# Optimization experiments

Measured on AMD Instinct MI355X. Metric: run time of the kernel, lower is better.

Reference implementation:

```python
import jax, jax.numpy as jnp
import numpy as np

B, S, D, H, DH, F = 2, 2048, 1024, 16, 64, 4096
EPS = 1e-5


def layernorm(x, gamma, beta):
    mu = jnp.mean(x, axis=-1, keepdims=True)
    var = jnp.mean((x - mu) ** 2, axis=-1, keepdims=True)
    return (x - mu) * jax.lax.rsqrt(var + EPS) * gamma + beta


def setup_inputs() -> dict:
    key = jax.random.key(0)
    ks = jax.random.split(key, 13)
    sc = 0.02
    return {
        "x": jax.random.normal(ks[0], (B, S, D), jnp.float32),
        "W_Q": jax.random.normal(ks[1], (H, DH, D), jnp.float32) * sc,  # per-head [d_head, d_model]
        "W_K": jax.random.normal(ks[2], (H, DH, D), jnp.float32) * sc,
        "W_V": jax.random.normal(ks[3], (H, DH, D), jnp.float32) * sc,
        "W_O": jax.random.normal(ks[4], (H * DH, D), jnp.float32) * sc,
        "W_up": jax.random.normal(ks[5], (D, F), jnp.float32) * sc,
        "b_up": jax.random.normal(ks[6], (F,), jnp.float32) * sc,
        "W_down": jax.random.normal(ks[7], (F, D), jnp.float32) * sc,
        "b_down": jax.random.normal(ks[8], (D,), jnp.float32) * sc,
        "gamma_1": jnp.ones((D,), jnp.float32),
        "beta_1": jnp.zeros((D,), jnp.float32),
        "gamma_2": jnp.ones((D,), jnp.float32),
        "beta_2": jnp.zeros((D,), jnp.float32),
    }


def reference(x, W_Q, W_K, W_V, W_O, W_up, b_up, W_down, b_down, gamma_1, beta_1, gamma_2, beta_2):
    u = layernorm(x, gamma_1, beta_1)
    # per-head projections: input @ W.t() -> [B, H, S, DH]
    Q = jnp.einsum("bsd,hed->bhse", u, W_Q)
    K = jnp.einsum("bsd,hed->bhse", u, W_K)
    V = jnp.einsum("bsd,hed->bhse", u, W_V)
    # Faithful quirk: original does K.reshape(B, DH, S) (raw reshape, NOT transpose)
    K_r = K.reshape(B, H, DH, S)
    scores = jnp.matmul(Q, K_r) / D  # [B,H,S,S]; quirk: scaled by d_model, not sqrt(d_head)
    attn = jax.nn.softmax(scores, axis=-1)
    heads = jnp.matmul(attn, V)  # [B,H,S,DH]
    heads_cat = heads.transpose(0, 2, 1, 3).reshape(B, S, H * DH)  # concat heads on last dim
    z1 = x + heads_cat @ W_O
    v1 = layernorm(z1, gamma_2, beta_2)
    v3 = jax.nn.gelu(v1 @ W_up + b_up, approximate=False)
    z2 = z1 + v3 @ W_down + b_down
    return z2
```

## Files before the change

### kernel.cpp

```cpp
#include <hip/hip_runtime.h>
#include <hip/hip_bf16.h>


typedef __attribute__((ext_vector_type(8))) short short8v;
typedef __attribute__((ext_vector_type(4))) short short4v;
typedef __attribute__((ext_vector_type(4))) float f32x4;

__device__ __forceinline__ float b2f(unsigned short u) {
    unsigned int x = ((unsigned int)u) << 16;
    float f;
    __builtin_memcpy(&f, &x, 4);
    return f;
}
__device__ __forceinline__ unsigned short f2b(float f) {
    unsigned int x;
    __builtin_memcpy(&x, &f, 4);
    unsigned int r = (x + 0x7FFFu + ((x >> 16) & 1u)) >> 16;
    return (unsigned short)r;
}
__device__ __forceinline__ void gload16(const unsigned short* g, unsigned short* l) {
    __builtin_amdgcn_global_load_lds(
        (const __attribute__((address_space(1))) unsigned int*)g,
        (__attribute__((address_space(3))) unsigned int*)l, 16, 0, 0);
}
__device__ __forceinline__ bool is_f32(const unsigned int* flagp) {
    return *flagp == 0x3F800000u;
}

__global__ __launch_bounds__(256) void cast_qkv_k(const void* __restrict__ s0,
                                                  const void* __restrict__ s1,
                                                  const void* __restrict__ s2,
                                                  unsigned short* __restrict__ dst,
                                                  const unsigned int* __restrict__ flagp) {
    const bool f32 = is_f32(flagp);
    const int seg = blockIdx.x >> 9;
    const int i = ((blockIdx.x & 511) * 256 + threadIdx.x) * 8;
    const void* src = seg == 0 ? s0 : (seg == 1 ? s1 : s2);
    unsigned short* d = dst + (size_t)seg * 1048576 + i;
    if (f32) {
        const float* s = (const float*)src + i;
        float4 a = *(const float4*)s;
        float4 b = *(const float4*)(s + 4);
        union { unsigned short u[8]; int4 v; } o;
        o.u[0] = f2b(a.x); o.u[1] = f2b(a.y); o.u[2] = f2b(a.z); o.u[3] = f2b(a.w);
        o.u[4] = f2b(b.x); o.u[5] = f2b(b.y); o.u[6] = f2b(b.z); o.u[7] = f2b(b.w);
        *(int4*)d = o.v;
    } else {
        *(int4*)d = *(const int4*)((const unsigned short*)src + i);
    }
}

__global__ __launch_bounds__(256) void cast_small_k(const void* __restrict__ s0,
                                                    const void* __restrict__ s1,
                                                    const void* __restrict__ s2,
                                                    const void* __restrict__ s3,
                                                    const void* __restrict__ s4,
                                                    const void* __restrict__ s5,
                                                    unsigned short* __restrict__ dst,
                                                    const unsigned int* __restrict__ flagp) {
    const bool f32 = is_f32(flagp);
    const int seg = blockIdx.x < 2 ? 0 : blockIdx.x - 1;
    const void* srcs[6] = {s0, s1, s2, s3, s4, s5};
    const int offs[6] = {0, 4096, 5120, 6144, 7168, 8192};
    const int lens[6] = {4096, 1024, 1024, 1024, 1024, 1024};
    const int base = (blockIdx.x < 2 ? blockIdx.x * 2048 : 0);
    const int i = base + threadIdx.x * 8;
    if (i >= lens[seg]) return;
    const void* src = srcs[seg];
    unsigned short* d = dst + offs[seg] + i;
    if (f32) {
        const float* s = (const float*)src + i;
        float4 a = *(const float4*)s;
        float4 b = *(const float4*)(s + 4);
        union { unsigned short u[8]; int4 v; } o;
        o.u[0] = f2b(a.x); o.u[1] = f2b(a.y); o.u[2] = f2b(a.z); o.u[3] = f2b(a.w);
        o.u[4] = f2b(b.x); o.u[5] = f2b(b.y); o.u[6] = f2b(b.z); o.u[7] = f2b(b.w);
        *(int4*)d = o.v;
    } else {
        *(int4*)d = *(const int4*)((const unsigned short*)src + i);
    }
}

__global__ __launch_bounds__(256) void castT_k(const void* __restrict__ src,
                                               unsigned short* __restrict__ dst,
                                               int rows, int cols,
                                               const unsigned int* __restrict__ flagp) {
    const bool f32 = is_f32(flagp);
    __shared__ float tile[32][33];
    const int t = threadIdx.x, tx = t & 31, ty = t >> 5;
    const int c0 = blockIdx.x * 32, r0 = blockIdx.y * 32;
#pragma unroll
    for (int i = 0; i < 4; i++) {
        int r = r0 + ty + i * 8;
        float v;
        if (f32) v = ((const float*)src)[(size_t)r * cols + c0 + tx];
        else     v = b2f(((const unsigned short*)src)[(size_t)r * cols + c0 + tx]);
        tile[ty + i * 8][tx] = v;
    }
    __syncthreads();
#pragma unroll
    for (int i = 0; i < 4; i++) {
        int c = c0 + ty + i * 8;
        dst[(size_t)c * rows + r0 + tx] = f2b(tile[tx][ty + i * 8]);
    }
}

__global__ __launch_bounds__(256) void kvT_k(const unsigned short* __restrict__ Kn,
                                             const unsigned short* __restrict__ Vn,
                                             unsigned short* __restrict__ Ktt,
                                             unsigned short* __restrict__ Vtt) {
    __shared__ unsigned short tile[64][72];
    const int blk = blockIdx.x;
    const int bh = blk >> 6;
    const int sub = blk & 63;
    const size_t base = (size_t)bh * (2048 * 64);
    const unsigned short* src;
    unsigned short* dst;
    int R, C, r0, c0;
    if (sub < 32) { src = Kn + base; dst = Ktt + base; R = 64;   C = 2048; r0 = 0;              c0 = sub * 64; }
    else          { src = Vn + base; dst = Vtt + base; R = 2048; C = 64;   r0 = (sub - 32) * 64; c0 = 0; }
    const int t = threadIdx.x;
    const int tx = t & 7, ty = t >> 3;
#pragma unroll
    for (int i = 0; i < 2; i++) {
        int r = ty + i * 32;
        union { int4 v; unsigned short u[8]; } ld;
        ld.v = *(const int4*)&src[(size_t)(r0 + r) * C + c0 + tx * 8];
#pragma unroll
        for (int k = 0; k < 8; k++) tile[tx * 8 + k][r] = ld.u[k];
    }
    __syncthreads();
#pragma unroll
    for (int i = 0; i < 2; i++) {
        int c = ty + i * 32;
        union { int4 v; unsigned short u[8]; } stv;
#pragma unroll
        for (int k = 0; k < 8; k++) stv.u[k] = tile[c][tx * 8 + k];
        *(int4*)&dst[(size_t)(c0 + c) * R + r0 + tx * 8] = stv.v;
    }
}

__global__ __launch_bounds__(256) void fin_k(const float* __restrict__ src,
                                             const unsigned short* __restrict__ P0,
                                             const unsigned short* __restrict__ P1,
                                             void* __restrict__ dst,
                                             const unsigned short* __restrict__ bias,
                                             const unsigned int* __restrict__ flagp) {
    const bool f32 = is_f32(flagp);
    const int i = (blockIdx.x * 256 + threadIdx.x) * 4;
    float4 v = *(const float4*)(src + i);
    uint2 p0 = *(const uint2*)(P0 + i);
    uint2 p1 = *(const uint2*)(P1 + i);
    int c = i & 1023;
    v.x += b2f(bias[c])     + b2f((unsigned short)(p0.x & 0xffff)) + b2f((unsigned short)(p1.x & 0xffff));
    v.y += b2f(bias[c + 1]) + b2f((unsigned short)(p0.x >> 16))    + b2f((unsigned short)(p1.x >> 16));
    v.z += b2f(bias[c + 2]) + b2f((unsigned short)(p0.y & 0xffff)) + b2f((unsigned short)(p1.y & 0xffff));
    v.w += b2f(bias[c + 3]) + b2f((unsigned short)(p0.y >> 16))    + b2f((unsigned short)(p1.y >> 16));
    if (f32) {
        *(float4*)((float*)dst + i) = v;
    } else {
        union { unsigned short u[4]; uint2 q; } o;
        o.u[0] = f2b(v.x); o.u[1] = f2b(v.y); o.u[2] = f2b(v.z); o.u[3] = f2b(v.w);
        *(uint2*)((unsigned short*)dst + i) = o.q;
    }
}

template <int MODE>
__global__ __launch_bounds__(256) void ln_k(const void* __restrict__ inp,
                                            unsigned short* __restrict__ outp,
                                            const unsigned short* __restrict__ gamma,
                                            const unsigned short* __restrict__ beta,
                                            const unsigned int* __restrict__ flagp) {
    const int row = blockIdx.x, t = threadIdx.x;
    float xv[4];
    bool f32 = (MODE == 1) ? true : is_f32(flagp);
    if (f32) {
        const float* p = (const float*)inp + (size_t)row * 1024 + t * 4;
        float4 v = *(const float4*)p;
        xv[0] = v.x; xv[1] = v.y; xv[2] = v.z; xv[3] = v.w;
    } else {
        const unsigned short* p = (const unsigned short*)inp + (size_t)row * 1024 + t * 4;
        uint2 v = *(const uint2*)p;
        xv[0] = b2f((unsigned short)(v.x & 0xffff));
        xv[1] = b2f((unsigned short)(v.x >> 16));
        xv[2] = b2f((unsigned short)(v.y & 0xffff));
        xv[3] = b2f((unsigned short)(v.y >> 16));
    }
    float s = xv[0] + xv[1] + xv[2] + xv[3];
    float q = xv[0] * xv[0] + xv[1] * xv[1] + xv[2] * xv[2] + xv[3] * xv[3];
#pragma unroll
    for (int off = 32; off >= 1; off >>= 1) {
        s += __shfl_xor(s, off);
        q += __shfl_xor(q, off);
    }
    __shared__ float ls[8];
    if ((t & 63) == 0) { ls[t >> 6] = s; ls[4 + (t >> 6)] = q; }
    __syncthreads();
    s = ls[0] + ls[1] + ls[2] + ls[3];
    q = ls[4] + ls[5] + ls[6] + ls[7];
    const float mu = s * (1.f / 1024.f);
    const float rs = rsqrtf(q * (1.f / 1024.f) - mu * mu + 1e-5f);
    union { unsigned short u[4]; uint2 v; } o;
#pragma unroll
    for (int i = 0; i < 4; i++) {
        int c = t * 4 + i;
        o.u[i] = f2b((xv[i] - mu) * rs * b2f(gamma[c]) + b2f(beta[c]));
    }
    *(uint2*)(outp + (size_t)row * 1024 + t * 4) = o.v;
}

template <int EPI>
__global__ __launch_bounds__(256) void gemm_k(const unsigned short* __restrict__ A,
                                              const unsigned short* __restrict__ Bm,
                                              unsigned short* __restrict__ C,
                                              unsigned short* __restrict__ C2,
                                              unsigned short* __restrict__ C3,
                                              const unsigned short* __restrict__ bias,
                                              float* __restrict__ outf,
                                              const void* __restrict__ xres,
                                              const unsigned int* __restrict__ flagp,
                                              int N, int ldk, int tilesM, int tilesN,
                                              int kLen) {
    __shared__ unsigned short As[2][128 * 32];
    __shared__ unsigned short Bs[2][128 * 32];
    const int t = threadIdx.x;
    const int w = t >> 6, lane = t & 63, ln = t & 15, quad = (t & 63) >> 4;
    const int wm = w >> 1, wn = w & 1;
    const int bm = blockIdx.x % tilesM;
    const int bn = (blockIdx.x / tilesM) % tilesN;
    const int kc = blockIdx.x / (tilesM * tilesN);
    const int m0 = bm << 7, n0 = bn << 7;
    const int k0 = kc * kLen;
    f32x4 acc[4][4] = {};

    const int srow = lane >> 2;
    const int scol = (lane & 3) << 3;

    const size_t arow[2] = {(size_t)(m0 + (0 * 4 + w) * 16 + srow) * ldk + scol,
                            (size_t)(m0 + (1 * 4 + w) * 16 + srow) * ldk + scol};
    const size_t brow[2] = {(size_t)(n0 + (0 * 4 + w) * 16 + srow) * ldk + scol,
                            (size_t)(n0 + (1 * 4 + w) * 16 + srow) * ldk + scol};

#pragma unroll
    for (int r = 0; r < 2; r++) {
        const int blk = r * 4 + w;
        gload16(&A[arow[r] + k0], &As[0][blk * 512]);
        gload16(&Bm[brow[r] + k0], &Bs[0][blk * 512]);
    }

    int cur = 0;
    for (int kt = k0; kt < k0 + kLen; kt += 32) {
        asm volatile("s_waitcnt vmcnt(0)" ::: "memory");
        __syncthreads();
        if (kt + 32 < k0 + kLen) {
#pragma unroll
            for (int r = 0; r < 2; r++) {
                const int blk = r * 4 + w;
                gload16(&A[arow[r] + kt + 32], &As[cur ^ 1][blk * 512]);
                gload16(&Bm[brow[r] + kt + 32], &Bs[cur ^ 1][blk * 512]);
            }
        }
        short8v af[4], bfv[4];
#pragma unroll
        for (int mi = 0; mi < 4; mi++)
            af[mi] = *(const short8v*)&As[cur][(wm * 64 + mi * 16 + ln) * 32 + quad * 8];
#pragma unroll
        for (int nj = 0; nj < 4; nj++)
            bfv[nj] = *(const short8v*)&Bs[cur][(wn * 64 + nj * 16 + ln) * 32 + quad * 8];
#pragma unroll
        for (int mi = 0; mi < 4; mi++)
#pragma unroll
            for (int nj = 0; nj < 4; nj++)
                acc[mi][nj] = __builtin_amdgcn_mfma_f32_16x16x32_bf16(
                    af[mi], bfv[nj], acc[mi][nj], 0, 0, 0);
        cur ^= 1;
    }

    bool xf32 = false;
    if (EPI == 3) xf32 = is_f32(flagp);
    unsigned short* Cp = C;
    if (EPI == 8) Cp = C + (size_t)kc * 4194304;

#pragma unroll
    for (int mi = 0; mi < 4; mi++) {
#pragma unroll
        for (int nj = 0; nj < 4; nj++) {
#pragma unroll
            for (int r = 0; r < 4; r++) {
                const int m = m0 + wm * 64 + mi * 16 + quad * 4 + r;
                const int n = n0 + wn * 64 + nj * 16 + ln;
                float v = acc[mi][nj][r];
                if (EPI == 3) {
                    float xv = xf32 ? ((const float*)xres)[(size_t)m * N + n]
                                    : b2f(((const unsigned short*)xres)[(size_t)m * N + n]);
                    outf[(size_t)m * N + n] = v + xv;
                } else if (EPI == 4) {
                    float x = v + b2f(bias[n]);
                    C[(size_t)m * N + n] = f2b(0.5f * x * (1.f + erff(x * 0.70710678118654752f)));
                } else if (EPI == 6) {
                    int b = m >> 11, s = m & 2047;
                    int seg = n >> 10, nn = n & 1023, h = nn >> 6, e = nn & 63;
                    size_t off = ((size_t)(b * 16 + h) * 2048 + s) * 64 + e;
                    if (seg == 0)      C[off]  = f2b(v);
                    else if (seg == 1) C2[off] = f2b(v);
                    else               C3[off] = f2b(v);
                } else {
                    Cp[(size_t)m * N + n] = f2b(v);
                }
            }
        }
    }
}

__global__ __launch_bounds__(512, 4) void attn_k(const unsigned short* __restrict__ Q,
                                                 const unsigned short* __restrict__ Kt,
                                                 const unsigned short* __restrict__ Vt,
                                                 unsigned short* __restrict__ Hd) {
    __shared__ unsigned short Ks[2][2][128 * 32];
    __shared__ unsigned short Vs[2][64 * 128];
    const int t = threadIdx.x;
    const int w = t >> 6, l = t & 63, ln = t & 15, quad = (t & 63) >> 4;
    const int qt = blockIdx.x & 15, bh = blockIdx.x >> 4;
    const int b = bh >> 4, h = bh & 15;
    const int i0 = qt << 7;

    short8v aq[2];
    {
        const unsigned short* qp =
            Q + ((size_t)bh * 2048 + i0 + w * 16 + ln) * 64 + quad * 8;
        aq[0] = *(const short8v*)qp;
        aq[1] = *(const short8v*)(qp + 32);
    }

    const size_t kbase = (size_t)bh * (2048 * 64);
    const size_t vbase = (size_t)bh * (64 * 2048);

    size_t ksrc[2]; int klds[2];
    size_t vsrc[2]; int vlds[2];
#pragma unroll
    for (int r = 0; r < 2; r++) {
        int idx2 = w * 2 + r;
        int ksp = idx2 & 1, J = idx2 >> 1;
        ksrc[r] = (size_t)(J * 16 + (l >> 2)) * 64 + ksp * 32 + (l & 3) * 8;
        klds[r] = ksp * 4096 + J * 512;
        int c = idx2;
        int e = c * 4 + (l >> 4), pp = l & 15;
        int g = (pp & 8) | ((pp & 7) ^ (e & 7));
        vsrc[r] = (size_t)e * 2048 + g * 8;
        vlds[r] = c * 512;
    }

#pragma unroll
    for (int r = 0; r < 2; r++) {
        gload16(Kt + kbase + ksrc[r], &Ks[0][0][0] + klds[r]);
        gload16(Vt + vbase + vsrc[r], &Vs[0][0] + vlds[r]);
    }

    f32x4 O[4] = {};
    float lsum = 0.f;
    int cur = 0;
    const float sc = 9.765625e-4f;

    for (int jt = 0; jt < 16; jt++) {
        asm volatile("s_waitcnt vmcnt(0)" ::: "memory");
        __syncthreads();
        if (jt < 15) {
            const size_t j1 = (size_t)(jt + 1) << 7;
#pragma unroll
            for (int r = 0; r < 2; r++) {
                gload16(Kt + kbase + j1 * 64 + ksrc[r], &Ks[cur ^ 1][0][0] + klds[r]);
                gload16(Vt + vbase + j1 + vsrc[r], &Vs[cur ^ 1][0] + vlds[r]);
            }
        }

        f32x4 S[8] = {};
#pragma unroll
        for (int ks = 0; ks < 2; ks++) {
#pragma unroll
            for (int nj = 0; nj < 8; nj++) {
                short8v bk = *(const short8v*)&Ks[cur][ks][(nj * 16 + ln) * 32 + quad * 8];
                S[nj] = __builtin_amdgcn_mfma_f32_16x16x32_bf16(bk, aq[ks], S[nj], 0, 0, 0);
            }
        }
        short4v pk[8];
#pragma unroll
        for (int nj = 0; nj < 8; nj++) {
            union { unsigned short u[4]; short4v v; } pu;
#pragma unroll
            for (int r = 0; r < 4; r++) {
                float p = __expf(S[nj][r] * sc);
                lsum += p;
                pu.u[r] = f2b(p);
            }
            pk[nj] = pu.v;
        }
#pragma unroll
        for (int nj = 0; nj < 8; nj++) {
            int g = 2 * nj + (quad >> 1);
            int pos = (g & 8) | ((g & 7) ^ (ln & 7));
            int off = pos * 8 + (quad & 1) * 4;
#pragma unroll
            for (int ne = 0; ne < 4; ne++) {
                short4v bv = *(const short4v*)&Vs[cur][(ne * 16 + ln) * 128 + off];
                O[ne] = __builtin_amdgcn_mfma_f32_16x16x16bf16_1k(pk[nj], bv, O[ne], 0, 0, 0);
            }
        }
        cur ^= 1;
    }

    lsum += __shfl_xor(lsum, 16);
    lsum += __shfl_xor(lsum, 32);

#pragma unroll
    for (int r = 0; r < 4; r++) {
        float lr = __shfl(lsum, quad * 4 + r);
        float inv = 1.f / lr;
#pragma unroll
        for (int ne = 0; ne < 4; ne++) {
            int i = i0 + w * 16 + quad * 4 + r;
            int e = ne * 16 + ln;
            Hd[((size_t)(b * 2048 + i)) * 1024 + h * 64 + e] = f2b(O[ne][r] * inv);
        }
    }
}

extern "C" void kernel_launch(void* const* d_in, const int* in_sizes, int n_in,
                              void* d_out, int out_size, void* d_ws, size_t ws_size,
                              hipStream_t stream) {
    const unsigned int* flagp = (const unsigned int*)d_in[9];

    unsigned short* p = (unsigned short*)d_ws;
    unsigned short* Wqkv  = p; p += 3145728;
    unsigned short* WOt   = p; p += 1048576;
    unsigned short* Wupt  = p; p += 4194304;
    unsigned short* Wdnt  = p; p += 4194304;
    unsigned short* smallv = p; p += 9216;
    unsigned short* u     = p; p += 4194304;
    unsigned short* Qn    = p; p += 4194304;
    unsigned short* Kn    = p; p += 4194304;
    unsigned short* Vn    = p; p += 4194304;
    unsigned short* Ktt   = p; p += 4194304;
    unsigned short* Vtt   = p; p += 4194304;
    unsigned short* hd    = p; p += 4194304;
    float*          z1    = (float*)p;
    unsigned short* bupc = smallv;
    unsigned short* bdnc = smallv + 4096;
    unsigned short* g1c  = smallv + 5120;
    unsigned short* be1c = smallv + 6144;
    unsigned short* g2c  = smallv + 7168;
    unsigned short* be2c = smallv + 8192;
    unsigned short* v1   = u;
    unsigned short* v3   = Qn;
    unsigned short* Pd   = Wqkv;

    dim3 blk(256);
    cast_qkv_k<<<1536, blk, 0, stream>>>(d_in[1], d_in[2], d_in[3], Wqkv, flagp);
    castT_k<<<dim3(32, 32),  blk, 0, stream>>>(d_in[4], WOt,  1024, 1024, flagp);
    castT_k<<<dim3(128, 32), blk, 0, stream>>>(d_in[5], Wupt, 1024, 4096, flagp);
    castT_k<<<dim3(32, 128), blk, 0, stream>>>(d_in[7], Wdnt, 4096, 1024, flagp);
    cast_small_k<<<7, blk, 0, stream>>>(d_in[6], d_in[8], d_in[9], d_in[10], d_in[11],
                                        d_in[12], smallv, flagp);

    ln_k<0><<<4096, blk, 0, stream>>>(d_in[0], u, g1c, be1c, flagp);
    gemm_k<6><<<768, blk, 0, stream>>>(u, Wqkv, Qn, Kn, Vn, nullptr, nullptr,
                                       nullptr, nullptr, 3072, 1024, 32, 24, 1024);
    kvT_k<<<2048, blk, 0, stream>>>(Kn, Vn, Ktt, Vtt);
    attn_k<<<512, dim3(512), 0, stream>>>(Qn, Ktt, Vtt, hd);
    gemm_k<3><<<256, blk, 0, stream>>>(hd, WOt, nullptr, nullptr, nullptr, nullptr, z1,
                                       d_in[0], flagp, 1024, 1024, 32, 8, 1024);
    ln_k<1><<<4096, blk, 0, stream>>>(z1, v1, g2c, be2c, flagp);
    gemm_k<4><<<1024, blk, 0, stream>>>(v1, Wupt, v3, nullptr, nullptr, bupc, nullptr,
                                        nullptr, nullptr, 4096, 1024, 32, 32, 1024);
    gemm_k<8><<<512, blk, 0, stream>>>(v3, Wdnt, Pd, nullptr, nullptr, nullptr, nullptr,
                                       nullptr, nullptr, 1024, 4096, 32, 8, 2048);
    fin_k<<<4096, blk, 0, stream>>>(z1, Pd, Pd + 4194304, d_out, bdnc, flagp);
}
```

Baseline: 412.8 us.

## Add 256x256-tile GEMM with 4-stage LDS pipeline for QKV, up and down projections

Adds a new gemm256_k kernel with 512 threads and 256x256 output tiles. It uses a 4-buffer direct-to-LDS prefetch ring with explicit waitcnt and barrier scheduling, swizzled LDS reads, and raised wave priority around the MFMA blocks. It replaces the 128x128 GEMMs for the QKV, FFN-up and FFN-down projections to raise data reuse per tile. The down projection now splits K four ways instead of two, so fin_k sums four bf16 partial buffers that reuse dead scratch regions. The costs are lower grid counts (192–256 blocks) and higher LDS and register pressure, with a risk of poor CU fill.

```diff
diff --git a/kernel.cpp b/kernel.cpp
--- a/kernel.cpp
+++ b/kernel.cpp
@@ -143,6 +143,8 @@
 __global__ __launch_bounds__(256) void fin_k(const float* __restrict__ src,
                                              const unsigned short* __restrict__ P0,
                                              const unsigned short* __restrict__ P1,
+                                             const unsigned short* __restrict__ P2,
+                                             const unsigned short* __restrict__ P3,
                                              void* __restrict__ dst,
                                              const unsigned short* __restrict__ bias,
                                              const unsigned int* __restrict__ flagp) {
@@ -151,11 +153,17 @@
     float4 v = *(const float4*)(src + i);
     uint2 p0 = *(const uint2*)(P0 + i);
     uint2 p1 = *(const uint2*)(P1 + i);
+    uint2 p2 = *(const uint2*)(P2 + i);
+    uint2 p3 = *(const uint2*)(P3 + i);
     int c = i & 1023;
-    v.x += b2f(bias[c])     + b2f((unsigned short)(p0.x & 0xffff)) + b2f((unsigned short)(p1.x & 0xffff));
-    v.y += b2f(bias[c + 1]) + b2f((unsigned short)(p0.x >> 16))    + b2f((unsigned short)(p1.x >> 16));
-    v.z += b2f(bias[c + 2]) + b2f((unsigned short)(p0.y & 0xffff)) + b2f((unsigned short)(p1.y & 0xffff));
-    v.w += b2f(bias[c + 3]) + b2f((unsigned short)(p0.y >> 16))    + b2f((unsigned short)(p1.y >> 16));
+    v.x += b2f(bias[c])     + b2f((unsigned short)(p0.x & 0xffff)) + b2f((unsigned short)(p1.x & 0xffff))
+                            + b2f((unsigned short)(p2.x & 0xffff)) + b2f((unsigned short)(p3.x & 0xffff));
+    v.y += b2f(bias[c + 1]) + b2f((unsigned short)(p0.x >> 16))    + b2f((unsigned short)(p1.x >> 16))
+                            + b2f((unsigned short)(p2.x >> 16))    + b2f((unsigned short)(p3.x >> 16));
+    v.z += b2f(bias[c + 2]) + b2f((unsigned short)(p0.y & 0xffff)) + b2f((unsigned short)(p1.y & 0xffff))
+                            + b2f((unsigned short)(p2.y & 0xffff)) + b2f((unsigned short)(p3.y & 0xffff));
+    v.w += b2f(bias[c + 3]) + b2f((unsigned short)(p0.y >> 16))    + b2f((unsigned short)(p1.y >> 16))
+                            + b2f((unsigned short)(p2.y >> 16))    + b2f((unsigned short)(p3.y >> 16));
     if (f32) {
         *(float4*)((float*)dst + i) = v;
     } else {
@@ -278,8 +286,6 @@
 
     bool xf32 = false;
     if (EPI == 3) xf32 = is_f32(flagp);
-    unsigned short* Cp = C;
-    if (EPI == 8) Cp = C + (size_t)kc * 4194304;
 
 #pragma unroll
     for (int mi = 0; mi < 4; mi++) {
@@ -294,9 +300,133 @@
                     float xv = xf32 ? ((const float*)xres)[(size_t)m * N + n]
                                     : b2f(((const unsigned short*)xres)[(size_t)m * N + n]);
                     outf[(size_t)m * N + n] = v + xv;
-                } else if (EPI == 4) {
+                }
+            }
+        }
+    }
+}
+
+template <int EPI>
+__global__ __launch_bounds__(512, 2) void gemm256_k(const unsigned short* __restrict__ A,
+                                                    const unsigned short* __restrict__ Bm,
+                                                    unsigned short* __restrict__ C,
+                                                    unsigned short* __restrict__ C2,
+                                                    unsigned short* __restrict__ C3,
+                                                    const unsigned short* __restrict__ bias,
+                                                    int N, int ldk, int tilesM, int tilesN,
+                                                    int kLen) {
+    __shared__ unsigned short As[4][8192];
+    __shared__ unsigned short Bs[4][8192];
+    const int t = threadIdx.x;
+    const int w = t >> 6, l = t & 63, ln = t & 15, quad = (t & 63) >> 4;
+    const int wm = w >> 2, wn = w & 3;
+
+    const int nwg = gridDim.x;
+    const int wg = ((int)blockIdx.x & 7) * (nwg >> 3) + ((int)blockIdx.x >> 3);
+
+    const int bm = wg % tilesM;
+    const int bn = (wg / tilesM) % tilesN;
+    const int kc = wg / (tilesM * tilesN);
+    const int m0 = bm << 8, n0 = bn << 8;
+    const int k0 = kc * kLen;
+    const int nk = kLen >> 5;
+
+    const int lrow = l >> 2;
+    const int lswz = (((l & 3) ^ (lrow & 3)) << 3);
+    const size_t aG0 = (size_t)(m0 + (w << 4) + lrow) * ldk + k0 + lswz;
+    const size_t aG1 = aG0 + ((size_t)ldk << 7);
+    const size_t bG0 = (size_t)(n0 + (w << 4) + lrow) * ldk + k0 + lswz;
+    const size_t bG1 = bG0 + ((size_t)ldk << 7);
+    const int ldsLo = w * 512;
+    const int ldsHi = 4096 + w * 512;
+
+    const int swz8 = ((quad ^ (ln & 3)) << 3);
+    const int raBase = (wm * 128 + ln) * 32 + swz8;
+    const int rbBase = (wn * 64 + ln) * 32 + swz8;
+
+    f32x4 acc[8][4] = {};
+
+    gload16(&A[aG0], &As[0][ldsLo]);
+    gload16(&Bm[bG0], &Bs[0][ldsLo]);
+    gload16(&A[aG1], &As[0][ldsHi]);
+    gload16(&Bm[bG1], &Bs[0][ldsHi]);
+    if (nk > 1) {
+        gload16(&A[aG0 + 32], &As[1][ldsLo]);
+        gload16(&Bm[bG0 + 32], &Bs[1][ldsLo]);
+        gload16(&A[aG1 + 32], &As[1][ldsHi]);
+        gload16(&Bm[bG1 + 32], &Bs[1][ldsHi]);
+    }
+
+    for (int tI = 0; tI < nk; ++tI) {
+        const int buf = tI & 3;
+        if (tI + 1 < nk) {
+            asm volatile("s_waitcnt vmcnt(4)" ::: "memory");
+        } else {
+            asm volatile("s_waitcnt vmcnt(0)" ::: "memory");
+        }
+        __builtin_amdgcn_sched_barrier(0);
+        __builtin_amdgcn_s_barrier();
+        asm volatile("" ::: "memory");
+        __builtin_amdgcn_sched_barrier(0);
+
+        const unsigned short* Ab = As[buf];
+        const unsigned short* Bb = Bs[buf];
+        const int nb = (tI + 2) & 3;
+        const size_t ko = (size_t)(tI + 2) << 5;
+
+        if (tI + 2 < nk) {
+            gload16(&A[aG0 + ko], &As[nb][ldsLo]);
+            gload16(&Bm[bG0 + ko], &Bs[nb][ldsLo]);
+        }
+        short8v bf[4], af[4];
+#pragma unroll
+        for (int nj = 0; nj < 4; nj++) bf[nj] = *(const short8v*)&Bb[rbBase + nj * 512];
+#pragma unroll
+        for (int mi = 0; mi < 4; mi++) af[mi] = *(const short8v*)&Ab[raBase + mi * 512];
+        asm volatile("s_waitcnt lgkmcnt(0)" ::: "memory");
+        __builtin_amdgcn_sched_barrier(0);
+        __builtin_amdgcn_s_setprio(1);
+#pragma unroll
+        for (int mi = 0; mi < 4; mi++)
+#pragma unroll
+            for (int nj = 0; nj < 4; nj++)
+                acc[mi][nj] = __builtin_amdgcn_mfma_f32_16x16x32_bf16(
+                    af[mi], bf[nj], acc[mi][nj], 0, 0, 0);
+        __builtin_amdgcn_s_setprio(0);
+
+        if (tI + 2 < nk) {
+            gload16(&A[aG1 + ko], &As[nb][ldsHi]);
+            gload16(&Bm[bG1 + ko], &Bs[nb][ldsHi]);
+        }
+#pragma unroll
+        for (int mi = 0; mi < 4; mi++) af[mi] = *(const short8v*)&Ab[raBase + (mi + 4) * 512];
+        asm volatile("s_waitcnt lgkmcnt(0)" ::: "memory");
+        __builtin_amdgcn_sched_barrier(0);
+        __builtin_amdgcn_s_setprio(1);
+#pragma unroll
+        for (int mi = 0; mi < 4; mi++)
+#pragma unroll
+            for (int nj = 0; nj < 4; nj++)
+                acc[mi + 4][nj] = __builtin_amdgcn_mfma_f32_16x16x32_bf16(
+                    af[mi], bf[nj], acc[mi + 4][nj], 0, 0, 0);
+        __builtin_amdgcn_s_setprio(0);
+    }
+
+    unsigned short* Cp = C;
+    if (EPI == 8) Cp = (kc == 0) ? C : (kc == 1) ? (C + 4194304) : (kc == 2) ? C2 : C3;
+
+#pragma unroll
+    for (int mi = 0; mi < 8; mi++) {
+#pragma unroll
+        for (int nj = 0; nj < 4; nj++) {
+#pragma unroll
+            for (int r = 0; r < 4; r++) {
+                const int m = m0 + wm * 128 + mi * 16 + quad * 4 + r;
+                const int n = n0 + wn * 64 + nj * 16 + ln;
+                float v = acc[mi][nj][r];
+                if (EPI == 4) {
                     float x = v + b2f(bias[n]);
-                    C[(size_t)m * N + n] = f2b(0.5f * x * (1.f + erff(x * 0.70710678118654752f)));
+                    Cp[(size_t)m * N + n] = f2b(0.5f * x * (1.f + erff(x * 0.70710678118654752f)));
                 } else if (EPI == 6) {
                     int b = m >> 11, s = m & 2047;
                     int seg = n >> 10, nn = n & 1023, h = nn >> 6, e = nn & 63;
@@ -451,7 +581,9 @@
     unsigned short* be2c = smallv + 8192;
     unsigned short* v1   = u;
     unsigned short* v3   = Qn;
-    unsigned short* Pd   = Wqkv;
+    unsigned short* Pd0  = Wqkv;
+    unsigned short* Pd2  = Vtt;
+    unsigned short* Pd3  = hd;
 
     dim3 blk(256);
     cast_qkv_k<<<1536, blk, 0, stream>>>(d_in[1], d_in[2], d_in[3], Wqkv, flagp);
@@ -462,16 +594,16 @@
                                         d_in[12], smallv, flagp);
 
     ln_k<0><<<4096, blk, 0, stream>>>(d_in[0], u, g1c, be1c, flagp);
-    gemm_k<6><<<768, blk, 0, stream>>>(u, Wqkv, Qn, Kn, Vn, nullptr, nullptr,
-                                       nullptr, nullptr, 3072, 1024, 32, 24, 1024);
+    gemm256_k<6><<<192, dim3(512), 0, stream>>>(u, Wqkv, Qn, Kn, Vn, nullptr,
+                                                3072, 1024, 16, 12, 1024);
     kvT_k<<<2048, blk, 0, stream>>>(Kn, Vn, Ktt, Vtt);
     attn_k<<<512, dim3(512), 0, stream>>>(Qn, Ktt, Vtt, hd);
     gemm_k<3><<<256, blk, 0, stream>>>(hd, WOt, nullptr, nullptr, nullptr, nullptr, z1,
                                        d_in[0], flagp, 1024, 1024, 32, 8, 1024);
     ln_k<1><<<4096, blk, 0, stream>>>(z1, v1, g2c, be2c, flagp);
-    gemm_k<4><<<1024, blk, 0, stream>>>(v1, Wupt, v3, nullptr, nullptr, bupc, nullptr,
-                                        nullptr, nullptr, 4096, 1024, 32, 32, 1024);
-    gemm_k<8><<<512, blk, 0, stream>>>(v3, Wdnt, Pd, nullptr, nullptr, nullptr, nullptr,
-                                       nullptr, nullptr, 1024, 4096, 32, 8, 2048);
-    fin_k<<<4096, blk, 0, stream>>>(z1, Pd, Pd + 4194304, d_out, bdnc, flagp);
-}
+    gemm256_k<4><<<256, dim3(512), 0, stream>>>(v1, Wupt, v3, nullptr, nullptr, bupc,
+                                                4096, 1024, 16, 16, 1024);
+    gemm256_k<8><<<256, dim3(512), 0, stream>>>(v3, Wdnt, Pd0, Pd2, Pd3, nullptr,
+                                                1024, 4096, 16, 4, 1024);
+    fin_k<<<4096, blk, 0, stream>>>(z1, Pd0, Pd0 + 4194304, Pd2, Pd3, d_out, bdnc, flagp);
+}
```

After: 412.7 us. No clear change (-0.0%).
